# Optimization experiments

Hardware: AMD Instinct MI355X
Metric: run time of the kernel (lower is better)

## Reference

```python
import jax, jax.numpy as jnp
import numpy as np

B, C, D, N, K = 2, 64, 3, 4096, 16
E = 2 * C      # edge-feature channels (128)
H = 2 * E      # expansion hidden channels (256)


def setup_inputs() -> dict:
    key = jax.random.key(0)
    ks = jax.random.split(key, 7)
    s1 = 1.0 / np.sqrt(E).astype(np.float32)
    s2 = 1.0 / np.sqrt(H).astype(np.float32)
    return {
        "x":  jax.random.normal(ks[0], (B, C, D, N), jnp.float32),
        "W1": jax.random.normal(ks[1], (H, E), jnp.float32) * s1,
        "b1": jax.random.normal(ks[2], (H,), jnp.float32) * s1,
        "W2": jax.random.normal(ks[3], (H, H), jnp.float32) * s2,
        "b2": jax.random.normal(ks[4], (H,), jnp.float32) * s2,
        "W3": jax.random.normal(ks[5], (C, H), jnp.float32) * s2,
        "b3": jax.random.normal(ks[6], (C,), jnp.float32) * s2,
    }


def _knn_idx(pc, k):
    """pc: (B, C, N). Returns (B, k, N) indices of k nearest neighbors
    (self excluded), matching KNN(ref=pc, query=pc) then idx[:, 1:, :]."""
    sq = jnp.sum(pc * pc, axis=1)                                  # (B, N)
    d2 = sq[:, :, None] - 2.0 * jnp.einsum('bcn,bcm->bnm', pc, pc) + sq[:, None, :]
    _, idx = jax.lax.top_k(-d2, k + 1)                             # (B, N, k+1) nearest-first
    return jnp.transpose(idx[:, :, 1:], (0, 2, 1))                 # drop self -> (B, k, N)


def reference(x, W1, b1, W2, b2, W3, b3):
    mean_pc = jnp.mean(x, axis=2)                                  # (B, C, N)
    idx = _knn_idx(mean_pc, K)                                     # (B, K, N), int32
    # grouping_operation: out[b,c,k,n] = mean_pc[b, c, idx[b,k,n]]
    nbr = jax.vmap(lambda f, i: f[:, i])(mean_pc, idx)             # (B, C, K, N)
    central = jnp.broadcast_to(x[:, :, None, :, :], (B, C, K, D, N))
    nbr_e = jnp.broadcast_to(nbr[:, :, :, None, :], (B, C, K, D, N))
    edge = jnp.concatenate([central, nbr_e - central], axis=1)     # (B, 2C, K, D, N)
    bc = lambda b: b[None, :, None, None, None]
    h = jax.nn.relu(jnp.einsum('oi,bikdn->bokdn', W1, edge) + bc(b1))
    h = jax.nn.relu(jnp.einsum('oi,bikdn->bokdn', W2, h) + bc(b2))
    r = jnp.einsum('oi,bikdn->bokdn', W3, h) + bc(b3)              # (B, C, K, D, N)
    return jnp.max(r, axis=2) + x                                  # (B, C, D, N)
```

## Files before the change

### kernel.cpp

```cpp
#include <hip/hip_runtime.h>

typedef unsigned short u16;
typedef float f32x4 __attribute__((ext_vector_type(4)));
typedef short bf16x8 __attribute__((ext_vector_type(8)));
typedef u16 u16x4 __attribute__((ext_vector_type(4)));
typedef unsigned int uint2v __attribute__((ext_vector_type(2)));


static __device__ __forceinline__ u16 f2bf(float x) {
    union { float f; unsigned int u; } v; v.f = x;
    unsigned int u = v.u;
    unsigned int r = u + 0x7fffu + ((u >> 16) & 1u);
    return (u16)(r >> 16);
}

static __device__ __forceinline__ float bf2f(u16 h) {
    union { unsigned int u; float f; } v; v.u = ((unsigned int)h) << 16;
    return v.f;
}

static __device__ __forceinline__ unsigned int pk2(float a, float b) {
    return (unsigned int)f2bf(a) | ((unsigned int)f2bf(b) << 16);
}

__global__ __launch_bounds__(256) void mean_kernel(const float* __restrict__ x,
                                                   float* __restrict__ pc) {
    int t = blockIdx.x * 256 + threadIdx.x;
    int n = t & 4095;
    int bc = t >> 12;
    const float* xp = x + bc * 3 * 4096 + n;
    pc[t] = (xp[0] + xp[4096] + xp[8192]) / 3.0f;
}

__global__ __launch_bounds__(256) void sq_kernel(const float* __restrict__ pc,
                                                 float* __restrict__ sq) {
    int t = blockIdx.x * 256 + threadIdx.x;
    int b = t >> 12, n = t & 4095;
    float s = 0.f;
    #pragma unroll
    for (int c = 0; c < 64; ++c) {
        float v = pc[(b * 64 + c) * 4096 + n];
        s += v * v;
    }
    sq[t] = s;
}

#define INSERT(dist, idxv) do { \
    float _v = (dist); int _vi = (idxv); \
    _Pragma("unroll") \
    for (int _s = 0; _s < 16; ++_s) { \
        bool _c = _v < bd[_s]; \
        float _nb = _c ? _v : bd[_s]; \
        float _nv = _c ? bd[_s] : _v; \
        int _nbi = _c ? _vi : bi[_s]; \
        int _nvi = _c ? bi[_s] : _vi; \
        bd[_s] = _nb; _v = _nv; bi[_s] = _nbi; _vi = _nvi; \
    } } while (0)

__global__ __launch_bounds__(256, 3) void knn_part_kernel(const float* __restrict__ pc,
                                                          const float* __restrict__ sq,
                                                          float* __restrict__ pd,
                                                          int* __restrict__ pi) {
    __shared__ float ptile[64][128];
    __shared__ float sqt[128];
    int tid = threadIdx.x;
    int bid = blockIdx.x;
    int ch = bid & 31, qb = (bid >> 5) & 15, b = bid >> 9;
    int n = qb * 256 + tid;
    int m0 = ch * 128;

    #pragma unroll
    for (int it = 0; it < 8; ++it) {
        int lin4 = it * 256 + tid;
        int c = lin4 >> 5, mm4 = (lin4 & 31) * 4;
        *(float4*)&ptile[c][mm4] =
            *(const float4*)&pc[(b * 64 + c) * 4096 + m0 + mm4];
    }
    if (tid < 128) sqt[tid] = sq[b * 4096 + m0 + tid];

    float qv[64];
    #pragma unroll
    for (int c = 0; c < 64; ++c) qv[c] = pc[(b * 64 + c) * 4096 + n];
    float sqn = sq[b * 4096 + n];

    float bd[16]; int bi[16];
    #pragma unroll
    for (int s = 0; s < 16; ++s) { bd[s] = 3.4e38f; bi[s] = -1; }
    __syncthreads();

    for (int mb = 0; mb < 128; mb += 4) {
        float d0 = 0.f, d1 = 0.f, d2 = 0.f, d3 = 0.f;
        #pragma unroll
        for (int c = 0; c < 64; ++c) {
            float4 pv = *(const float4*)&ptile[c][mb];
            float qc = qv[c];
            d0 = fmaf(qc, pv.x, d0);
            d1 = fmaf(qc, pv.y, d1);
            d2 = fmaf(qc, pv.z, d2);
            d3 = fmaf(qc, pv.w, d3);
        }
        int m = m0 + mb;
        float e0 = (sqn - 2.f * d0) + sqt[mb + 0]; if (m + 0 == n) e0 = 3.4e38f;
        float e1 = (sqn - 2.f * d1) + sqt[mb + 1]; if (m + 1 == n) e1 = 3.4e38f;
        float e2 = (sqn - 2.f * d2) + sqt[mb + 2]; if (m + 2 == n) e2 = 3.4e38f;
        float e3 = (sqn - 2.f * d3) + sqt[mb + 3]; if (m + 3 == n) e3 = 3.4e38f;
        INSERT(e0, m + 0);
        INSERT(e1, m + 1);
        INSERT(e2, m + 2);
        INSERT(e3, m + 3);
    }
    int base = ((b * 4096 + n) * 32 + ch) * 16;
    #pragma unroll
    for (int s = 0; s < 16; ++s) { pd[base + s] = bd[s]; pi[base + s] = bi[s]; }
}

__global__ __launch_bounds__(256) void knn_merge_kernel(const float* __restrict__ pd,
                                                        const int* __restrict__ pi,
                                                        int* __restrict__ idxw) {
    int tid = threadIdx.x;
    int lane = tid & 63;
    int q = blockIdx.x * 4 + (tid >> 6);
    int base = q * 512;

    float d[8]; int ix[8];
    #pragma unroll
    for (int j = 0; j < 8; ++j) {
        d[j] = pd[base + lane + 64 * j];
        ix[j] = pi[base + lane + 64 * j];
    }

    for (int e = 0; e < 16; ++e) {
        float lmd = d[0]; int lmi = ix[0];
        #pragma unroll
        for (int j = 1; j < 8; ++j) {
            bool c = d[j] < lmd;
            lmd = c ? d[j] : lmd;
            lmi = c ? ix[j] : lmi;
        }
        float wm = lmd;
        #pragma unroll
        for (int off = 32; off; off >>= 1)
            wm = fminf(wm, __shfl_xor(wm, off));
        unsigned long long msk = __ballot(lmd == wm);
        int L = (int)__ffsll(msk) - 1;
        int wmi = __shfl(lmi, L);
        if (lane == 0) idxw[q * 16 + e] = wmi;
        if (lane == L) {
            #pragma unroll
            for (int j = 0; j < 8; ++j)
                if (ix[j] == wmi) d[j] = 3.4e38f;
        }
    }
}

__global__ __launch_bounds__(256) void prep_kernel(const float* __restrict__ W1,
                                                   const float* __restrict__ W2,
                                                   const float* __restrict__ W3,
                                                   u16* __restrict__ W2bf,
                                                   u16* __restrict__ W3bf,
                                                   float* __restrict__ W1dT,
                                                   float* __restrict__ W1bT) {
    int t = blockIdx.x * 256 + threadIdx.x;
    W2bf[t] = f2bf(W2[t]);
    if (t < 16384) {
        W3bf[t] = f2bf(W3[t]);
        int c = t >> 8, h = t & 255;
        float wa = W1[h * 128 + c];
        float wb = W1[h * 128 + 64 + c];
        W1dT[t] = wa - wb;
        W1bT[t] = wb;
    }
}

__global__ __launch_bounds__(256) void q_kernel(const float* __restrict__ pc,
                                               const float* __restrict__ W1bT,
                                               u16* __restrict__ Qbf) {
    int h = threadIdx.x;
    int bid = blockIdx.x;
    int b = bid >> 10, m0 = (bid & 1023) * 4;
    float a0 = 0.f, a1 = 0.f, a2 = 0.f, a3 = 0.f;
    for (int c = 0; c < 64; ++c) {
        float w = W1bT[c * 256 + h];
        float4 pv = *(const float4*)(pc + (b * 64 + c) * 4096 + m0);
        a0 = fmaf(w, pv.x, a0);
        a1 = fmaf(w, pv.y, a1);
        a2 = fmaf(w, pv.z, a2);
        a3 = fmaf(w, pv.w, a3);
    }
    int ob = (b * 4096 + m0) * 256 + h;
    Qbf[ob] = f2bf(a0); Qbf[ob + 256] = f2bf(a1);
    Qbf[ob + 512] = f2bf(a2); Qbf[ob + 768] = f2bf(a3);
}

__global__ __launch_bounds__(256) void p_kernel(const float* __restrict__ x,
                                               const float* __restrict__ W1dT,
                                               const float* __restrict__ b1,
                                               u16* __restrict__ Pbf) {
    int h = threadIdx.x;
    int bid = blockIdx.x;
    int b = bid / 3072;
    int rem = bid % 3072;
    int d = rem >> 10;
    int n0 = (rem & 1023) * 4;
    float bias = b1[h];
    float a0 = bias, a1 = bias, a2 = bias, a3 = bias;
    for (int c = 0; c < 64; ++c) {
        float w = W1dT[c * 256 + h];
        float4 xv = *(const float4*)(x + ((b * 64 + c) * 3 + d) * 4096 + n0);
        a0 = fmaf(w, xv.x, a0);
        a1 = fmaf(w, xv.y, a1);
        a2 = fmaf(w, xv.z, a2);
        a3 = fmaf(w, xv.w, a3);
    }
    int ob = ((b * 3 + d) * 4096 + n0) * 256 + h;
    Pbf[ob] = f2bf(a0); Pbf[ob + 256] = f2bf(a1);
    Pbf[ob + 512] = f2bf(a2); Pbf[ob + 768] = f2bf(a3);
}

__global__ __launch_bounds__(256) void fused_mlp_kernel(const float* __restrict__ x,
                                                        const u16* __restrict__ Pbf,
                                                        const u16* __restrict__ Qbf,
                                                        const int* __restrict__ idxw,
                                                        const u16* __restrict__ W2bf,
                                                        const u16* __restrict__ W3bf,
                                                        const float* __restrict__ b2,
                                                        const float* __restrict__ b3,
                                                        float* __restrict__ out) {
    __shared__ u16 hL[96][264];

    int tid = threadIdx.x;
    int bid = blockIdx.x;
    int b = bid >> 11;
    int n0 = (bid & 2047) * 2;

    int w = tid >> 6, lane = tid & 63;

    {
        int g = w & 1, kh = (w >> 1) * 8;
        int n = n0 + g;
        u16x4 pv[3];
        #pragma unroll
        for (int d = 0; d < 3; ++d)
            pv[d] = *(const u16x4*)&Pbf[((b * 3 + d) * 4096 + n) * 256 + lane * 4];
        const int* idq = idxw + (b * 4096 + n) * 16 + kh;
        #pragma unroll
        for (int kk = 0; kk < 8; ++kk) {
            int m = idq[kk];
            u16x4 qv = *(const u16x4*)&Qbf[(b * 4096 + m) * 256 + lane * 4];
            float q0 = bf2f(qv[0]), q1 = bf2f(qv[1]), q2 = bf2f(qv[2]), q3 = bf2f(qv[3]);
            #pragma unroll
            for (int d = 0; d < 3; ++d) {
                uint2v hv;
                hv[0] = pk2(fmaxf(bf2f(pv[d][0]) + q0, 0.f), fmaxf(bf2f(pv[d][1]) + q1, 0.f));
                hv[1] = pk2(fmaxf(bf2f(pv[d][2]) + q2, 0.f), fmaxf(bf2f(pv[d][3]) + q3, 0.f));
                *(uint2v*)&hL[g * 48 + d * 16 + kh + kk][lane * 4] = hv;
            }
        }
    }
    __syncthreads();

    int cl = lane & 15, q = lane >> 4;

    f32x4 acc[4][6];
    #pragma unroll
    for (int i = 0; i < 4; ++i)
        #pragma unroll
        for (int jt = 0; jt < 6; ++jt)
            acc[i][jt] = (f32x4){0.f, 0.f, 0.f, 0.f};

    const u16* Arow = W2bf + (w * 64 + cl) * 256 + q * 8;
    for (int kt = 0; kt < 8; ++kt) {
        int k0 = kt * 32;
        bf16x8 a[4], bb[6];
        #pragma unroll
        for (int i = 0; i < 4; ++i)
            a[i] = *(const bf16x8*)(Arow + i * 4096 + k0);
        #pragma unroll
        for (int jt = 0; jt < 6; ++jt)
            bb[jt] = *(const bf16x8*)(&hL[jt * 16 + cl][k0 + q * 8]);
        #pragma unroll
        for (int i = 0; i < 4; ++i)
            #pragma unroll
            for (int jt = 0; jt < 6; ++jt)
                acc[i][jt] = __builtin_amdgcn_mfma_f32_16x16x32_bf16(a[i], bb[jt], acc[i][jt], 0, 0, 0);
    }
    __syncthreads();

    #pragma unroll
    for (int i = 0; i < 4; ++i) {
        int rowb = w * 64 + i * 16 + q * 4;
        float4 bv = *(const float4*)(b2 + rowb);
        #pragma unroll
        for (int jt = 0; jt < 6; ++jt) {
            f32x4 v = acc[i][jt];
            uint2v hv;
            hv[0] = pk2(fmaxf(v[0] + bv.x, 0.f), fmaxf(v[1] + bv.y, 0.f));
            hv[1] = pk2(fmaxf(v[2] + bv.z, 0.f), fmaxf(v[3] + bv.w, 0.f));
            *(uint2v*)&hL[jt * 16 + cl][rowb] = hv;
        }
    }
    __syncthreads();

    f32x4 acc3[6];
    #pragma unroll
    for (int jt = 0; jt < 6; ++jt) acc3[jt] = (f32x4){0.f, 0.f, 0.f, 0.f};

    const u16* A3row = W3bf + (w * 16 + cl) * 256 + q * 8;
    for (int kt = 0; kt < 8; ++kt) {
        int k0 = kt * 32;
        bf16x8 a3 = *(const bf16x8*)(A3row + k0);
        #pragma unroll
        for (int jt = 0; jt < 6; ++jt) {
            bf16x8 bb = *(const bf16x8*)(&hL[jt * 16 + cl][k0 + q * 8]);
            acc3[jt] = __builtin_amdgcn_mfma_f32_16x16x32_bf16(a3, bb, acc3[jt], 0, 0, 0);
        }
    }

    int rowb = w * 16 + q * 4;
    float4 b3v = *(const float4*)(b3 + rowb);
    #pragma unroll
    for (int jt = 0; jt < 6; ++jt) {
        int g = jt / 3, d = jt % 3;
        int n = n0 + g;
        f32x4 v = acc3[jt];
        v[0] += b3v.x;
        v[1] += b3v.y;
        v[2] += b3v.z;
        v[3] += b3v.w;
        #pragma unroll
        for (int off = 1; off < 16; off <<= 1) {
            v[0] = fmaxf(v[0], __shfl_xor(v[0], off));
            v[1] = fmaxf(v[1], __shfl_xor(v[1], off));
            v[2] = fmaxf(v[2], __shfl_xor(v[2], off));
            v[3] = fmaxf(v[3], __shfl_xor(v[3], off));
        }
        if (cl == 0) {
            #pragma unroll
            for (int r = 0; r < 4; ++r) {
                int addr = ((b * 64 + rowb + r) * 3 + d) * 4096 + n;
                out[addr] = v[r] + x[addr];
            }
        }
    }
}

extern "C" void kernel_launch(void* const* d_in, const int* in_sizes, int n_in,
                              void* d_out, int out_size, void* d_ws, size_t ws_size,
                              hipStream_t stream) {
    (void)in_sizes; (void)n_in; (void)out_size; (void)ws_size;
    const float* x  = (const float*)d_in[0];
    const float* W1 = (const float*)d_in[1];
    const float* b1 = (const float*)d_in[2];
    const float* W2 = (const float*)d_in[3];
    const float* b2 = (const float*)d_in[4];
    const float* W3 = (const float*)d_in[5];
    const float* b3 = (const float*)d_in[6];
    float* out = (float*)d_out;

    char* ws = (char*)d_ws;
    float* pc   = (float*)(ws + 0);
    float* sq   = (float*)(ws + 2097152);
    int*   idxw = (int*)  (ws + 2129920);
    u16*   Qbf  = (u16*)  (ws + 2654208);
    u16*   Pbf  = (u16*)  (ws + 6848512);
    u16*   W2bf = (u16*)  (ws + 19431424);
    u16*   W3bf = (u16*)  (ws + 19562496);
    float* W1dT = (float*)(ws + 19595264);
    float* W1bT = (float*)(ws + 19660800);
    float* pd   = (float*)(ws + 2654208);
    int*   pi   = (int*)  (ws + 19726336);

    mean_kernel<<<2048, 256, 0, stream>>>(x, pc);
    sq_kernel<<<32, 256, 0, stream>>>(pc, sq);
    knn_part_kernel<<<1024, 256, 0, stream>>>(pc, sq, pd, pi);
    knn_merge_kernel<<<2048, 256, 0, stream>>>(pd, pi, idxw);
    prep_kernel<<<256, 256, 0, stream>>>(W1, W2, W3, W2bf, W3bf, W1dT, W1bT);
    q_kernel<<<2048, 256, 0, stream>>>(pc, W1bT, Qbf);
    p_kernel<<<6144, 256, 0, stream>>>(x, W1dT, b1, Pbf);
    fused_mlp_kernel<<<4096, 256, 0, stream>>>(x, Pbf, Qbf, idxw, W2bf, W3bf, b2, b3, out);
}
```

Before: 379.0 us.

## Fuse small kernels: fold norms into kNN, weight prep into mean, merge Q/P

```diff
diff --git a/kernel.cpp b/kernel.cpp
--- a/kernel.cpp
+++ b/kernel.cpp
@@ -24,25 +24,31 @@
 }
 
 __global__ __launch_bounds__(256) void mean_kernel(const float* __restrict__ x,
-                                                   float* __restrict__ pc) {
+                                                   float* __restrict__ pc,
+                                                   const float* __restrict__ W1,
+                                                   const float* __restrict__ W2,
+                                                   const float* __restrict__ W3,
+                                                   u16* __restrict__ W2bf,
+                                                   u16* __restrict__ W3bf,
+                                                   float* __restrict__ W1dT,
+                                                   float* __restrict__ W1bT) {
     int t = blockIdx.x * 256 + threadIdx.x;
     int n = t & 4095;
     int bc = t >> 12;
     const float* xp = x + bc * 3 * 4096 + n;
     pc[t] = (xp[0] + xp[4096] + xp[8192]) / 3.0f;
-}
-
-__global__ __launch_bounds__(256) void sq_kernel(const float* __restrict__ pc,
-                                                 float* __restrict__ sq) {
-    int t = blockIdx.x * 256 + threadIdx.x;
-    int b = t >> 12, n = t & 4095;
-    float s = 0.f;
-    #pragma unroll
-    for (int c = 0; c < 64; ++c) {
-        float v = pc[(b * 64 + c) * 4096 + n];
-        s += v * v;
-    }
-    sq[t] = s;
+
+    if (t < 65536) {
+        W2bf[t] = f2bf(W2[t]);
+        if (t < 16384) {
+            W3bf[t] = f2bf(W3[t]);
+            int c = t >> 8, h = t & 255;
+            float wa = W1[h * 128 + c];
+            float wb = W1[h * 128 + 64 + c];
+            W1dT[t] = wa - wb;
+            W1bT[t] = wb;
+        }
+    }
 }
 
 #define INSERT(dist, idxv) do { \
@@ -58,7 +64,6 @@
     } } while (0)
 
 __global__ __launch_bounds__(256, 3) void knn_part_kernel(const float* __restrict__ pc,
-                                                          const float* __restrict__ sq,
                                                           float* __restrict__ pd,
                                                           int* __restrict__ pi) {
     __shared__ float ptile[64][128];
@@ -76,12 +81,24 @@
         *(float4*)&ptile[c][mm4] =
             *(const float4*)&pc[(b * 64 + c) * 4096 + m0 + mm4];
     }
-    if (tid < 128) sqt[tid] = sq[b * 4096 + m0 + tid];
+    __syncthreads();
+    if (tid < 128) {
+        float s = 0.f;
+        #pragma unroll
+        for (int c = 0; c < 64; ++c) {
+            float v = ptile[c][tid];
+            s = fmaf(v, v, s);
+        }
+        sqt[tid] = s;
+    }
 
     float qv[64];
-    #pragma unroll
-    for (int c = 0; c < 64; ++c) qv[c] = pc[(b * 64 + c) * 4096 + n];
-    float sqn = sq[b * 4096 + n];
+    float sqn = 0.f;
+    #pragma unroll
+    for (int c = 0; c < 64; ++c) {
+        qv[c] = pc[(b * 64 + c) * 4096 + n];
+        sqn = fmaf(qv[c], qv[c], sqn);
+    }
 
     float bd[16]; int bi[16];
     #pragma unroll
@@ -153,68 +170,59 @@
     }
 }
 
-__global__ __launch_bounds__(256) void prep_kernel(const float* __restrict__ W1,
-                                                   const float* __restrict__ W2,
-                                                   const float* __restrict__ W3,
-                                                   u16* __restrict__ W2bf,
-                                                   u16* __restrict__ W3bf,
-                                                   float* __restrict__ W1dT,
-                                                   float* __restrict__ W1bT) {
-    int t = blockIdx.x * 256 + threadIdx.x;
-    W2bf[t] = f2bf(W2[t]);
-    if (t < 16384) {
-        W3bf[t] = f2bf(W3[t]);
-        int c = t >> 8, h = t & 255;
-        float wa = W1[h * 128 + c];
-        float wb = W1[h * 128 + 64 + c];
-        W1dT[t] = wa - wb;
-        W1bT[t] = wb;
-    }
-}
-
-__global__ __launch_bounds__(256) void q_kernel(const float* __restrict__ pc,
-                                               const float* __restrict__ W1bT,
-                                               u16* __restrict__ Qbf) {
+__global__ __launch_bounds__(256) void qp_kernel(const float* __restrict__ pc,
+                                                 const float* __restrict__ x,
+                                                 const float* __restrict__ W1bT,
+                                                 const float* __restrict__ W1dT,
+                                                 const float* __restrict__ b1,
+                                                 u16* __restrict__ Qbf,
+                                                 u16* __restrict__ Pbf) {
     int h = threadIdx.x;
     int bid = blockIdx.x;
-    int b = bid >> 10, m0 = (bid & 1023) * 4;
-    float a0 = 0.f, a1 = 0.f, a2 = 0.f, a3 = 0.f;
-    for (int c = 0; c < 64; ++c) {
-        float w = W1bT[c * 256 + h];
-        float4 pv = *(const float4*)(pc + (b * 64 + c) * 4096 + m0);
-        a0 = fmaf(w, pv.x, a0);
-        a1 = fmaf(w, pv.y, a1);
-        a2 = fmaf(w, pv.z, a2);
-        a3 = fmaf(w, pv.w, a3);
-    }
-    int ob = (b * 4096 + m0) * 256 + h;
-    Qbf[ob] = f2bf(a0); Qbf[ob + 256] = f2bf(a1);
-    Qbf[ob + 512] = f2bf(a2); Qbf[ob + 768] = f2bf(a3);
-}
-
-__global__ __launch_bounds__(256) void p_kernel(const float* __restrict__ x,
-                                               const float* __restrict__ W1dT,
-                                               const float* __restrict__ b1,
-                                               u16* __restrict__ Pbf) {
-    int h = threadIdx.x;
-    int bid = blockIdx.x;
-    int b = bid / 3072;
-    int rem = bid % 3072;
-    int d = rem >> 10;
-    int n0 = (rem & 1023) * 4;
-    float bias = b1[h];
-    float a0 = bias, a1 = bias, a2 = bias, a3 = bias;
-    for (int c = 0; c < 64; ++c) {
-        float w = W1dT[c * 256 + h];
-        float4 xv = *(const float4*)(x + ((b * 64 + c) * 3 + d) * 4096 + n0);
-        a0 = fmaf(w, xv.x, a0);
-        a1 = fmaf(w, xv.y, a1);
-        a2 = fmaf(w, xv.z, a2);
-        a3 = fmaf(w, xv.w, a3);
-    }
-    int ob = ((b * 3 + d) * 4096 + n0) * 256 + h;
-    Pbf[ob] = f2bf(a0); Pbf[ob + 256] = f2bf(a1);
-    Pbf[ob + 512] = f2bf(a2); Pbf[ob + 768] = f2bf(a3);
+    if (bid < 1024) {
+        int b = bid >> 9, m0 = (bid & 511) * 8;
+        float a0 = 0.f, a1 = 0.f, a2 = 0.f, a3 = 0.f;
+        float a4 = 0.f, a5 = 0.f, a6 = 0.f, a7 = 0.f;
+        for (int c = 0; c < 64; ++c) {
+            float w = W1bT[c * 256 + h];
+            const float* pr = pc + (b * 64 + c) * 4096 + m0;
+            float4 p0 = *(const float4*)pr;
+            float4 p1 = *(const float4*)(pr + 4);
+            a0 = fmaf(w, p0.x, a0); a1 = fmaf(w, p0.y, a1);
+            a2 = fmaf(w, p0.z, a2); a3 = fmaf(w, p0.w, a3);
+            a4 = fmaf(w, p1.x, a4); a5 = fmaf(w, p1.y, a5);
+            a6 = fmaf(w, p1.z, a6); a7 = fmaf(w, p1.w, a7);
+        }
+        int ob = (b * 4096 + m0) * 256 + h;
+        Qbf[ob] = f2bf(a0); Qbf[ob + 256] = f2bf(a1);
+        Qbf[ob + 512] = f2bf(a2); Qbf[ob + 768] = f2bf(a3);
+        Qbf[ob + 1024] = f2bf(a4); Qbf[ob + 1280] = f2bf(a5);
+        Qbf[ob + 1536] = f2bf(a6); Qbf[ob + 1792] = f2bf(a7);
+    } else {
+        int pb = bid - 1024;
+        int b = pb / 1536;
+        int rem = pb % 1536;
+        int d = rem >> 9;
+        int n0 = (rem & 511) * 8;
+        float bias = b1[h];
+        float a0 = bias, a1 = bias, a2 = bias, a3 = bias;
+        float a4 = bias, a5 = bias, a6 = bias, a7 = bias;
+        for (int c = 0; c < 64; ++c) {
+            float w = W1dT[c * 256 + h];
+            const float* xr = x + ((b * 64 + c) * 3 + d) * 4096 + n0;
+            float4 x0 = *(const float4*)xr;
+            float4 x1 = *(const float4*)(xr + 4);
+            a0 = fmaf(w, x0.x, a0); a1 = fmaf(w, x0.y, a1);
+            a2 = fmaf(w, x0.z, a2); a3 = fmaf(w, x0.w, a3);
+            a4 = fmaf(w, x1.x, a4); a5 = fmaf(w, x1.y, a5);
+            a6 = fmaf(w, x1.z, a6); a7 = fmaf(w, x1.w, a7);
+        }
+        int ob = ((b * 3 + d) * 4096 + n0) * 256 + h;
+        Pbf[ob] = f2bf(a0); Pbf[ob + 256] = f2bf(a1);
+        Pbf[ob + 512] = f2bf(a2); Pbf[ob + 768] = f2bf(a3);
+        Pbf[ob + 1024] = f2bf(a4); Pbf[ob + 1280] = f2bf(a5);
+        Pbf[ob + 1536] = f2bf(a6); Pbf[ob + 1792] = f2bf(a7);
+    }
 }
 
 __global__ __launch_bounds__(256) void fused_mlp_kernel(const float* __restrict__ x,
@@ -231,7 +239,8 @@
     int tid = threadIdx.x;
     int bid = blockIdx.x;
     int b = bid >> 11;
-    int n0 = (bid & 2047) * 2;
+    int rr = bid & 2047;
+    int n0 = (((rr & 7) << 8) | (rr >> 3)) << 1;
 
     int w = tid >> 6, lane = tid & 63;
 
@@ -359,7 +368,6 @@
 
     char* ws = (char*)d_ws;
     float* pc   = (float*)(ws + 0);
-    float* sq   = (float*)(ws + 2097152);
     int*   idxw = (int*)  (ws + 2129920);
     u16*   Qbf  = (u16*)  (ws + 2654208);
     u16*   Pbf  = (u16*)  (ws + 6848512);
@@ -370,12 +378,9 @@
     float* pd   = (float*)(ws + 2654208);
     int*   pi   = (int*)  (ws + 19726336);
 
-    mean_kernel<<<2048, 256, 0, stream>>>(x, pc);
-    sq_kernel<<<32, 256, 0, stream>>>(pc, sq);
-    knn_part_kernel<<<1024, 256, 0, stream>>>(pc, sq, pd, pi);
+    mean_kernel<<<2048, 256, 0, stream>>>(x, pc, W1, W2, W3, W2bf, W3bf, W1dT, W1bT);
+    knn_part_kernel<<<1024, 256, 0, stream>>>(pc, pd, pi);
     knn_merge_kernel<<<2048, 256, 0, stream>>>(pd, pi, idxw);
-    prep_kernel<<<256, 256, 0, stream>>>(W1, W2, W3, W2bf, W3bf, W1dT, W1bT);
-    q_kernel<<<2048, 256, 0, stream>>>(pc, W1bT, Qbf);
-    p_kernel<<<6144, 256, 0, stream>>>(x, W1dT, b1, Pbf);
+    qp_kernel<<<4096, 256, 0, stream>>>(pc, x, W1bT, W1dT, b1, Qbf, Pbf);
     fused_mlp_kernel<<<4096, 256, 0, stream>>>(x, Pbf, Qbf, idxw, W2bf, W3bf, b2, b3, out);
 }
```

Result: faster. 360.0 us (-5.0%).
